# Optimization experiments

Hardware: AMD Instinct MI355X
Metric: run time of the kernel (lower is better)

The kernel has to match this reference:

```python
import jax, jax.numpy as jnp
import numpy as np


def setup_inputs() -> dict:
    key = jax.random.key(0)
    ks = jax.random.split(key, 6)
    N, T, D, H = 256, 128, 512, 512
    x = jax.random.normal(ks[0], (N, T, D), dtype=jnp.float32)
    A = jax.random.normal(ks[1], (N, H, 4, 4), dtype=jnp.float32)
    Wx = jax.random.normal(ks[2], (D, 4 * H), dtype=jnp.float32) / np.sqrt(D)
    Wh = jax.random.normal(ks[3], (H, 4 * H), dtype=jnp.float32) / np.sqrt(H)
    Wattn = jax.random.normal(ks[4], (H, 4 * H), dtype=jnp.float32) / np.sqrt(H)
    b = jnp.zeros((4 * H,), dtype=jnp.float32)
    return {"x": x, "A": A, "Wx": Wx, "Wh": Wh, "Wattn": Wattn, "b": b}


def reference(x, A, Wx, Wh, Wattn, b):
    N, T, D = x.shape
    H = Wh.shape[0]
    A_flat = A.reshape(N, H, -1)  # (N, H, 16)
    h0 = A_flat.mean(axis=-1)     # mean over 4x4 grid
    c0 = h0
    inv_sqrt_H = 1.0 / np.sqrt(H).astype(np.float32)

    def step(carry, x_t):
        h, c = carry
        # scaled dot-product attention over the 16 spatial cells
        scores = jnp.einsum('nh,nhp->np', h, A_flat) * inv_sqrt_H  # (N, 16)
        w = jax.nn.softmax(scores, axis=-1)
        attn = jnp.einsum('nhp,np->nh', A_flat, w)                 # (N, H)
        a = x_t @ Wx + h @ Wh + attn @ Wattn + b                   # (N, 4H)
        a_i, a_f, a_o, a_g = jnp.split(a, 4, axis=1)
        i = jax.nn.sigmoid(a_i)
        f = jax.nn.sigmoid(a_f)
        o = jax.nn.sigmoid(a_o)
        g = jnp.tanh(a_g)
        c_next = f * c + i * g
        h_next = o * jnp.tanh(c_next)
        return (h_next, c_next), h_next

    _, hs = jax.lax.scan(step, (h0, c0), jnp.swapaxes(x, 0, 1))  # (T, N, H)
    return jnp.swapaxes(hs, 0, 1)  # (N, T, H)
```

## Files before the change

kernel.cpp:

```cpp
#include <hip/hip_runtime.h>
#include <math.h>

typedef unsigned short u16;
typedef _Float16 h16;
typedef _Float16 f16x8 __attribute__((ext_vector_type(8)));
typedef float f32x4 __attribute__((ext_vector_type(4)));

__device__ __forceinline__ float sigm(float x) { return 1.f / (1.f + expf(-x)); }


__global__ void k_pack_w(const float* __restrict__ Wx, const float* __restrict__ Wh,
                         h16* __restrict__ WhiS, h16* __restrict__ WloS) {
  unsigned idx = blockIdx.x * 256 + threadIdx.x;
  unsigned e = idx & 7, l = (idx >> 3) & 63, cf = (idx >> 9) & 1;
  unsigned t2 = idx >> 10;
  unsigned j = t2 >> 5, ks = t2 & 31;
  unsigned k = ks * 32 + ((l >> 4) << 3) + e;
  unsigned c32 = cf * 16 + (l & 15);
  unsigned acol = (c32 >> 3) * 512 + j * 8 + (c32 & 7);
  float v = (k < 512) ? Wx[(size_t)k * 2048 + acol]
                      : Wh[(size_t)(k - 512) * 2048 + acol];
  h16 hi = (h16)v;
  WhiS[idx] = hi;
  WloS[idx] = (h16)((v - (float)hi) * 4096.f);
}

__global__ __launch_bounds__(256) void k_m(const float* __restrict__ Af,
                                           const float* __restrict__ Wat,
                                           float* __restrict__ M2) {
  __shared__ float Alds[8192];
  const int tid = threadIdx.x;
  const int cb = blockIdx.x;
  const int n  = blockIdx.y;
  {
    const float4* src = (const float4*)(Af + (size_t)n * 8192);
    float4* dst = (float4*)Alds;
    for (int i = tid; i < 2048; i += 256) dst[i] = src[i];
  }
  __syncthreads();
  const int c0 = cb * 512 + tid * 2;
  float acc0[16], acc1[16];
#pragma unroll
  for (int p = 0; p < 16; ++p) { acc0[p] = 0.f; acc1[p] = 0.f; }
  for (int k = 0; k < 512; ++k) {
    float2 wv2 = *(const float2*)(Wat + (size_t)k * 2048 + c0);
    const float* ar = Alds + k * 16;
#pragma unroll
    for (int p = 0; p < 16; ++p) {
      acc0[p] += ar[p] * wv2.x;
      acc1[p] += ar[p] * wv2.y;
    }
  }
  float* o = M2 + ((size_t)n * 2048 + c0) * 16;
#pragma unroll
  for (int p = 0; p < 16; ++p) { o[p] = acc0[p]; o[16 + p] = acc1[p]; }
}

__global__ void k_xsplit(const float* __restrict__ x, h16* __restrict__ xhi,
                         h16* __restrict__ xlo) {
  size_t i = ((size_t)blockIdx.x * 256 + threadIdx.x) * 4;
  float4 v = *(const float4*)(x + i);
  union { h16 h[4]; uint2 u; } a, b;
  float vv[4] = {v.x, v.y, v.z, v.w};
#pragma unroll
  for (int e = 0; e < 4; ++e) {
    h16 hh = (h16)vv[e];
    a.h[e] = hh;
    b.h[e] = (h16)((vv[e] - (float)hh) * 4096.f);
  }
  *(uint2*)(xhi + i) = a.u;
  *(uint2*)(xlo + i) = b.u;
}

__global__ __launch_bounds__(512) void k_init(const float* __restrict__ Af,
                                              h16* __restrict__ hhi,
                                              h16* __restrict__ hlo,
                                              float* __restrict__ cst,
                                              float* __restrict__ sb0) {
  const int n = blockIdx.x, k = threadIdx.x;
  float Areg[16];
  const f32x4* A4 = (const f32x4*)(Af + (size_t)n * 8192 + k * 16);
#pragma unroll
  for (int q4 = 0; q4 < 4; ++q4) {
    f32x4 v = A4[q4];
#pragma unroll
    for (int e = 0; e < 4; ++e) Areg[q4 * 4 + e] = v[e];
  }
  float s = 0.f;
#pragma unroll
  for (int p = 0; p < 16; ++p) s += Areg[p];
  s *= 0.0625f;
  const int idx = n * 512 + k;
  cst[idx] = s;
  h16 hh = (h16)s;
  hhi[idx] = hh;
  hlo[idx] = (h16)((s - (float)hh) * 4096.f);
  float ps[16];
#pragma unroll
  for (int p = 0; p < 16; ++p) ps[p] = s * Areg[p];
#pragma unroll
  for (int m = 1; m <= 4; m <<= 1)
#pragma unroll
    for (int p = 0; p < 16; ++p) ps[p] += __shfl_xor(ps[p], m);
  if ((k & 7) == 0) {
    float* o = sb0 + ((size_t)n * 64 + (k >> 3)) * 16;
#pragma unroll
    for (int p = 0; p < 16; ++p) o[p] = ps[p];
  }
}

template<bool XPRE>
__global__ __launch_bounds__(512, 4) void k_step(
    const float* __restrict__ bv, const float* __restrict__ Af,
    const float* __restrict__ x, const h16* __restrict__ xhi, const h16* __restrict__ xlo,
    const h16* __restrict__ WhiS, const h16* __restrict__ WloS,
    const float* __restrict__ Mws,
    const float* __restrict__ sbR, float* __restrict__ sbW,
    h16* __restrict__ hhi, h16* __restrict__ hlo,
    float* __restrict__ cst, float* __restrict__ out, int t) {
  __shared__ float P[7 * 1056];
  __shared__ float wsh[32][17];

  const int tid = threadIdx.x;
  const int l = tid & 63, wv = tid >> 6;
  const int bid = blockIdx.x;
  const int g = bid >> 6;
  const int j = (bid & 7) * 8 + ((bid >> 3) & 7);
  const int n0 = g * 32;
  const int rA = n0 + (l & 15);
  const int klane = (l >> 4) * 8;

  {
    const int nS = tid >> 4, pS = tid & 15;
    const float* sr = sbR + ((size_t)(n0 + nS) * 64) * 16 + pS;
    float s = 0.f;
#pragma unroll 8
    for (int jj = 0; jj < 64; ++jj) s += sr[jj * 16];
    s *= 0.04419417382415922f;
    float m = s;
#pragma unroll
    for (int o = 8; o >= 1; o >>= 1) m = fmaxf(m, __shfl_xor(m, o, 16));
    float e = __expf(s - m);
    float se = e;
#pragma unroll
    for (int o = 8; o >= 1; o >>= 1) se += __shfl_xor(se, o, 16);
    wsh[nS][pS] = e / se;
  }

  const h16* whiJ = WhiS + (size_t)j * 32768;
  const h16* wloJ = WloS + (size_t)j * 32768;

  const int rC = tid >> 3, qC = tid & 7;
  const int colC = j * 8 + qC;
  const float b_i = bv[colC], b_f = bv[512 + colC], b_o = bv[1024 + colC],
              b_g = bv[1536 + colC];

  const int rb = t & 1, wb = rb ^ 1;
  const h16* hhiR = hhi + (size_t)rb * 131072;
  const h16* hloR = hlo + (size_t)rb * 131072;

  f32x4 acc1[2][2], acc2[2][2];
#pragma unroll
  for (int rt = 0; rt < 2; ++rt)
#pragma unroll
    for (int cf = 0; cf < 2; ++cf) {
      acc1[rt][cf] = (f32x4){0.f, 0.f, 0.f, 0.f};
      acc2[rt][cf] = (f32x4){0.f, 0.f, 0.f, 0.f};
    }

  auto kstep = [&](int ksg) {
    const f16x8 bh0 = *(const f16x8*)(whiJ + ((size_t)(ksg * 2 + 0) * 64 + l) * 8);
    const f16x8 bh1 = *(const f16x8*)(whiJ + ((size_t)(ksg * 2 + 1) * 64 + l) * 8);
    const f16x8 bl0 = *(const f16x8*)(wloJ + ((size_t)(ksg * 2 + 0) * 64 + l) * 8);
    const f16x8 bl1 = *(const f16x8*)(wloJ + ((size_t)(ksg * 2 + 1) * 64 + l) * 8);
    f16x8 Ah[2], Al[2];
    const int kg = ksg * 32;
    if (kg < 512) {
      const size_t base = ((size_t)rA * 128 + t) * 512 + kg + klane;
      if (XPRE) {
#pragma unroll
        for (int rt = 0; rt < 2; ++rt) {
          Ah[rt] = *(const f16x8*)(xhi + base + (size_t)rt * 1048576);
          Al[rt] = *(const f16x8*)(xlo + base + (size_t)rt * 1048576);
        }
      } else {
#pragma unroll
        for (int rt = 0; rt < 2; ++rt) {
          const float* xp = x + base + (size_t)rt * 1048576;
          f32x4 v0 = *(const f32x4*)xp, v1 = *(const f32x4*)(xp + 4);
          float vv[8] = {v0[0], v0[1], v0[2], v0[3], v1[0], v1[1], v1[2], v1[3]};
#pragma unroll
          for (int e = 0; e < 8; ++e) {
            h16 hh = (h16)vv[e];
            Ah[rt][e] = hh;
            Al[rt][e] = (h16)((vv[e] - (float)hh) * 4096.f);
          }
        }
      }
    } else {
      const size_t base = (size_t)rA * 512 + (kg - 512) + klane;
#pragma unroll
      for (int rt = 0; rt < 2; ++rt) {
        Ah[rt] = *(const f16x8*)(hhiR + base + rt * 8192);
        Al[rt] = *(const f16x8*)(hloR + base + rt * 8192);
      }
    }
#pragma unroll
    for (int rt = 0; rt < 2; ++rt) {
      acc1[rt][0] = __builtin_amdgcn_mfma_f32_16x16x32_f16(Ah[rt], bh0, acc1[rt][0], 0, 0, 0);
      acc1[rt][1] = __builtin_amdgcn_mfma_f32_16x16x32_f16(Ah[rt], bh1, acc1[rt][1], 0, 0, 0);
      acc2[rt][0] = __builtin_amdgcn_mfma_f32_16x16x32_f16(Al[rt], bh0, acc2[rt][0], 0, 0, 0);
      acc2[rt][1] = __builtin_amdgcn_mfma_f32_16x16x32_f16(Al[rt], bh1, acc2[rt][1], 0, 0, 0);
      acc2[rt][0] = __builtin_amdgcn_mfma_f32_16x16x32_f16(Ah[rt], bl0, acc2[rt][0], 0, 0, 0);
      acc2[rt][1] = __builtin_amdgcn_mfma_f32_16x16x32_f16(Ah[rt], bl1, acc2[rt][1], 0, 0, 0);
    }
  };

#pragma unroll
  for (int i = 0; i < 4; ++i) kstep(wv + 8 * i);

  float accf[2][2][4];
#pragma unroll
  for (int rt = 0; rt < 2; ++rt)
#pragma unroll
    for (int cf = 0; cf < 2; ++cf)
#pragma unroll
      for (int rg = 0; rg < 4; ++rg)
        accf[rt][cf][rg] = acc1[rt][cf][rg] + acc2[rt][cf][rg] * (1.f / 4096.f);

  auto publish = [&](int slot) {
#pragma unroll
    for (int rt = 0; rt < 2; ++rt)
#pragma unroll
      for (int cf = 0; cf < 2; ++cf)
#pragma unroll
        for (int rg = 0; rg < 4; ++rg)
          P[slot * 1056 + (rt * 16 + (l >> 4) * 4 + rg) * 33 + cf * 16 + (l & 15)] =
              accf[rt][cf][rg];
  };
  auto addin = [&](int slot) {
#pragma unroll
    for (int rt = 0; rt < 2; ++rt)
#pragma unroll
      for (int cf = 0; cf < 2; ++cf)
#pragma unroll
        for (int rg = 0; rg < 4; ++rg)
          accf[rt][cf][rg] +=
              P[slot * 1056 + (rt * 16 + (l >> 4) * 4 + rg) * 33 + cf * 16 + (l & 15)];
  };

  if (wv >= 4) publish(wv - 4);
  __syncthreads();
  if (wv < 4) addin(wv);
  if (wv == 2) publish(4);
  if (wv == 3) publish(5);
  __syncthreads();
  if (wv == 0) addin(4);
  if (wv == 1) { addin(5); publish(6); }
  __syncthreads();
  if (wv == 0) { addin(6); publish(0); }
  __syncthreads();

  if (tid < 256) {
    const float* Mr = Mws + ((size_t)(n0 + rC) * 2048 + colC) * 16;
    float am[4];
#pragma unroll
    for (int f = 0; f < 4; ++f) {
      const float* mp = Mr + (size_t)f * 8192;
      float s = 0.f;
#pragma unroll
      for (int p = 0; p < 16; ++p) s += wsh[rC][p] * mp[p];
      am[f] = s;
    }
    float ai = P[rC * 33 + qC] + am[0] + b_i;
    float af_ = P[rC * 33 + 8 + qC] + am[1] + b_f;
    float ao = P[rC * 33 + 16 + qC] + am[2] + b_o;
    float ag = P[rC * 33 + 24 + qC] + am[3] + b_g;
    float ig = sigm(ai), fg = sigm(af_), og = sigm(ao), gg = tanhf(ag);
    const size_t cix = (size_t)(n0 + rC) * 512 + colC;
    float c = cst[cix];
    float cn = fg * c + ig * gg;
    cst[cix] = cn;
    float hn = og * tanhf(cn);
    h16 hh = (h16)hn;
    hhi[(size_t)wb * 131072 + cix] = hh;
    hlo[(size_t)wb * 131072 + cix] = (h16)((hn - (float)hh) * 4096.f);
    out[((size_t)(n0 + rC) * 128 + t) * 512 + colC] = hn;

    float Areg[16];
    const f32x4* A4 = (const f32x4*)(Af + ((size_t)(n0 + rC) * 512 + colC) * 16);
#pragma unroll
    for (int q4 = 0; q4 < 4; ++q4) {
      f32x4 v = A4[q4];
#pragma unroll
      for (int e = 0; e < 4; ++e) Areg[q4 * 4 + e] = v[e];
    }
    float ps[16];
#pragma unroll
    for (int p = 0; p < 16; ++p) ps[p] = hn * Areg[p];
#pragma unroll
    for (int m = 1; m <= 4; m <<= 1)
#pragma unroll
      for (int p = 0; p < 16; ++p) ps[p] += __shfl_xor(ps[p], m);
    if (qC == 0) {
      float* o = sbW + ((size_t)(n0 + rC) * 64 + j) * 16;
#pragma unroll
      for (int p = 0; p < 16; ++p) o[p] = ps[p];
    }
  }
}


extern "C" void kernel_launch(void* const* d_in, const int* in_sizes, int n_in,
                              void* d_out, int out_size, void* d_ws, size_t ws_size,
                              hipStream_t stream) {
  (void)in_sizes; (void)n_in; (void)out_size;
  const float* x   = (const float*)d_in[0];
  const float* Af  = (const float*)d_in[1];
  const float* Wx  = (const float*)d_in[2];
  const float* Wh  = (const float*)d_in[3];
  const float* Wat = (const float*)d_in[4];
  const float* bv  = (const float*)d_in[5];
  float* out = (float*)d_out;

  char* ws = (char*)d_ws;
  size_t off = 0;
  auto alloc = [&](size_t nb) {
    char* p = ws + off; off = (off + nb + 255) & ~(size_t)255; return p;
  };
  h16*   WhiS = (h16*)alloc(2097152ull * 2);
  h16*   WloS = (h16*)alloc(2097152ull * 2);
  float* Mws  = (float*)alloc(8388608ull * 4);
  float* sb   = (float*)alloc(2ull * 262144 * 4);
  h16*   hhi  = (h16*)alloc(262144ull * 2);
  h16*   hlo  = (h16*)alloc(262144ull * 2);
  float* cst  = (float*)alloc(131072ull * 4);
  size_t base_end = off;
  h16* xhi = (h16*)alloc(16777216ull * 2);
  h16* xlo = (h16*)alloc(16777216ull * 2);
  bool xpre = (ws_size >= base_end + 2ull * 16777216ull * 2 + 4096);

  k_pack_w<<<8192, 256, 0, stream>>>(Wx, Wh, WhiS, WloS);
  k_m<<<dim3(4, 256), 256, 0, stream>>>(Af, Wat, Mws);
  k_init<<<256, 512, 0, stream>>>(Af, hhi, hlo, cst, sb);
  if (xpre) k_xsplit<<<16384, 256, 0, stream>>>(x, xhi, xlo);

  for (int t = 0; t < 128; ++t) {
    const float* sbR = sb + (size_t)(t & 1) * 262144;
    float* sbW = (float*)sb + (size_t)((t + 1) & 1) * 262144;
    if (xpre)
      k_step<true><<<512, 512, 0, stream>>>(bv, Af, x, xhi, xlo, WhiS, WloS, Mws,
                                            sbR, sbW, hhi, hlo, cst, out, t);
    else
      k_step<false><<<512, 512, 0, stream>>>(bv, Af, x, xhi, xlo, WhiS, WloS, Mws,
                                             sbR, sbW, hhi, hlo, cst, out, t);
  }
}
```

Baseline: 2.785 ms.

## Pre-swizzle x and h into MFMA fragment layout and use MFMA for attention projection

Stores the fp16 hi/lo splits of x and h in a fragment-major layout, so each lane of a k_step wave reads one contiguous 16-byte chunk and the wave reads one contiguous block, instead of strided row accesses. The k_m precompute of the attention projection is rewritten to use split-fp16 MFMA over a larger grid in place of scalar FMA loops. Writers in k_init, k_xsplit and the step epilogue now use the matching swizzled indices. The cost is more complex index arithmetic and a scattered 2-byte write pattern for h.

New measurement: 2.261 ms. 18.8% less time.

```diff
diff --git a/kernel.cpp b/kernel.cpp
--- a/kernel.cpp
+++ b/kernel.cpp
@@ -30,7 +30,7 @@
                                            float* __restrict__ M2) {
   __shared__ float Alds[8192];
   const int tid = threadIdx.x;
-  const int cb = blockIdx.x;
+  const int ct = blockIdx.x;
   const int n  = blockIdx.y;
   {
     const float4* src = (const float4*)(Af + (size_t)n * 8192);
@@ -38,43 +38,58 @@
     for (int i = tid; i < 2048; i += 256) dst[i] = src[i];
   }
   __syncthreads();
-  const int c0 = cb * 512 + tid * 2;
-  float acc0[16], acc1[16];
-#pragma unroll
-  for (int p = 0; p < 16; ++p) { acc0[p] = 0.f; acc1[p] = 0.f; }
-  for (int k = 0; k < 512; ++k) {
-    float2 wv2 = *(const float2*)(Wat + (size_t)k * 2048 + c0);
-    const float* ar = Alds + k * 16;
-#pragma unroll
-    for (int p = 0; p < 16; ++p) {
-      acc0[p] += ar[p] * wv2.x;
-      acc1[p] += ar[p] * wv2.y;
-    }
-  }
-  float* o = M2 + ((size_t)n * 2048 + c0) * 16;
-#pragma unroll
-  for (int p = 0; p < 16; ++p) { o[p] = acc0[p]; o[16 + p] = acc1[p]; }
-}
-
-__global__ void k_xsplit(const float* __restrict__ x, h16* __restrict__ xhi,
-                         h16* __restrict__ xlo) {
-  size_t i = ((size_t)blockIdx.x * 256 + threadIdx.x) * 4;
-  float4 v = *(const float4*)(x + i);
-  union { h16 h[4]; uint2 u; } a, b;
-  float vv[4] = {v.x, v.y, v.z, v.w};
-#pragma unroll
-  for (int e = 0; e < 4; ++e) {
+  const int l = tid & 63, w = tid >> 6;
+  const int col = ct * 64 + w * 16 + (l & 15);
+  const int lq = l >> 4;
+  f32x4 acc1 = {0.f, 0.f, 0.f, 0.f}, acc2 = {0.f, 0.f, 0.f, 0.f};
+  for (int k0 = 0; k0 < 512; k0 += 32) {
+    float av[8], wv[8];
+#pragma unroll
+    for (int e = 0; e < 8; ++e) av[e] = Alds[(k0 + lq * 8 + e) * 16 + (l & 15)];
+#pragma unroll
+    for (int e = 0; e < 8; ++e) wv[e] = Wat[(size_t)(k0 + lq * 8 + e) * 2048 + col];
+    f16x8 Ah, Al_, Bh, Bl;
+#pragma unroll
+    for (int e = 0; e < 8; ++e) {
+      h16 ah = (h16)av[e]; Ah[e] = ah; Al_[e] = (h16)((av[e] - (float)ah) * 4096.f);
+      h16 bh = (h16)wv[e]; Bh[e] = bh; Bl[e]  = (h16)((wv[e] - (float)bh) * 4096.f);
+    }
+    acc1 = __builtin_amdgcn_mfma_f32_16x16x32_f16(Ah, Bh, acc1, 0, 0, 0);
+    acc2 = __builtin_amdgcn_mfma_f32_16x16x32_f16(Al_, Bh, acc2, 0, 0, 0);
+    acc2 = __builtin_amdgcn_mfma_f32_16x16x32_f16(Ah, Bl, acc2, 0, 0, 0);
+  }
+  float4 o;
+  o.x = acc1[0] + acc2[0] * (1.f / 4096.f);
+  o.y = acc1[1] + acc2[1] * (1.f / 4096.f);
+  o.z = acc1[2] + acc2[2] * (1.f / 4096.f);
+  o.w = acc1[3] + acc2[3] * (1.f / 4096.f);
+  *(float4*)(M2 + ((size_t)n * 2048 + col) * 16 + lq * 4) = o;
+}
+
+__global__ void k_xsplit(const float* __restrict__ x, h16* __restrict__ xfhi,
+                         h16* __restrict__ xflo) {
+  unsigned tg = blockIdx.x * 256 + threadIdx.x;
+  unsigned l = tg & 63, rt = (tg >> 6) & 1, ksg = (tg >> 7) & 15;
+  unsigned g = (tg >> 11) & 7, t = tg >> 14;
+  int n = g * 32 + rt * 16 + (l & 15);
+  int k0 = ksg * 32 + (l >> 4) * 8;
+  const float* xp = x + ((size_t)n * 128 + t) * 512 + k0;
+  f32x4 v0 = *(const f32x4*)xp, v1 = *(const f32x4*)(xp + 4);
+  float vv[8] = {v0[0], v0[1], v0[2], v0[3], v1[0], v1[1], v1[2], v1[3]};
+  union { h16 h[8]; uint4 u; } a, b;
+#pragma unroll
+  for (int e = 0; e < 8; ++e) {
     h16 hh = (h16)vv[e];
     a.h[e] = hh;
     b.h[e] = (h16)((vv[e] - (float)hh) * 4096.f);
   }
-  *(uint2*)(xhi + i) = a.u;
-  *(uint2*)(xlo + i) = b.u;
+  *(uint4*)(xfhi + (size_t)tg * 8) = a.u;
+  *(uint4*)(xflo + (size_t)tg * 8) = b.u;
 }
 
 __global__ __launch_bounds__(512) void k_init(const float* __restrict__ Af,
-                                              h16* __restrict__ hhi,
-                                              h16* __restrict__ hlo,
+                                              h16* __restrict__ hfhi,
+                                              h16* __restrict__ hflo,
                                               float* __restrict__ cst,
                                               float* __restrict__ sb0) {
   const int n = blockIdx.x, k = threadIdx.x;
@@ -90,11 +105,13 @@
 #pragma unroll
   for (int p = 0; p < 16; ++p) s += Areg[p];
   s *= 0.0625f;
-  const int idx = n * 512 + k;
-  cst[idx] = s;
+  cst[n * 512 + k] = s;
   h16 hh = (h16)s;
-  hhi[idx] = hh;
-  hlo[idx] = (h16)((s - (float)hh) * 4096.f);
+  const int g = n >> 5;
+  const int hoff = ((((g * 16 + (k >> 5)) * 2 + ((n >> 4) & 1)) * 64 +
+                     ((n & 15) | (((k >> 3) & 3) << 4))) * 8) + (k & 7);
+  hfhi[hoff] = hh;
+  hflo[hoff] = (h16)((s - (float)hh) * 4096.f);
   float ps[16];
 #pragma unroll
   for (int p = 0; p < 16; ++p) ps[p] = s * Areg[p];
@@ -112,11 +129,11 @@
 template<bool XPRE>
 __global__ __launch_bounds__(512, 4) void k_step(
     const float* __restrict__ bv, const float* __restrict__ Af,
-    const float* __restrict__ x, const h16* __restrict__ xhi, const h16* __restrict__ xlo,
+    const float* __restrict__ x, const h16* __restrict__ xfhi, const h16* __restrict__ xflo,
     const h16* __restrict__ WhiS, const h16* __restrict__ WloS,
     const float* __restrict__ Mws,
     const float* __restrict__ sbR, float* __restrict__ sbW,
-    h16* __restrict__ hhi, h16* __restrict__ hlo,
+    h16* __restrict__ hfhi, h16* __restrict__ hflo,
     float* __restrict__ cst, float* __restrict__ out, int t) {
   __shared__ float P[7 * 1056];
   __shared__ float wsh[32][17];
@@ -127,8 +144,6 @@
   const int g = bid >> 6;
   const int j = (bid & 7) * 8 + ((bid >> 3) & 7);
   const int n0 = g * 32;
-  const int rA = n0 + (l & 15);
-  const int klane = (l >> 4) * 8;
 
   {
     const int nS = tid >> 4, pS = tid & 15;
@@ -156,8 +171,8 @@
               b_g = bv[1536 + colC];
 
   const int rb = t & 1, wb = rb ^ 1;
-  const h16* hhiR = hhi + (size_t)rb * 131072;
-  const h16* hloR = hlo + (size_t)rb * 131072;
+  const h16* hfhiR = hfhi + (size_t)rb * 131072;
+  const h16* hfloR = hflo + (size_t)rb * 131072;
 
   f32x4 acc1[2][2], acc2[2][2];
 #pragma unroll
@@ -174,19 +189,20 @@
     const f16x8 bl0 = *(const f16x8*)(wloJ + ((size_t)(ksg * 2 + 0) * 64 + l) * 8);
     const f16x8 bl1 = *(const f16x8*)(wloJ + ((size_t)(ksg * 2 + 1) * 64 + l) * 8);
     f16x8 Ah[2], Al[2];
-    const int kg = ksg * 32;
-    if (kg < 512) {
-      const size_t base = ((size_t)rA * 128 + t) * 512 + kg + klane;
+    if (ksg < 16) {
       if (XPRE) {
 #pragma unroll
         for (int rt = 0; rt < 2; ++rt) {
-          Ah[rt] = *(const f16x8*)(xhi + base + (size_t)rt * 1048576);
-          Al[rt] = *(const f16x8*)(xlo + base + (size_t)rt * 1048576);
+          const size_t base = ((((size_t)t * 8 + g) * 16 + ksg) * 2 + rt) * 512 + l * 8;
+          Ah[rt] = *(const f16x8*)(xfhi + base);
+          Al[rt] = *(const f16x8*)(xflo + base);
         }
       } else {
 #pragma unroll
         for (int rt = 0; rt < 2; ++rt) {
-          const float* xp = x + base + (size_t)rt * 1048576;
+          const int n_x = g * 32 + rt * 16 + (l & 15);
+          const int k_x = ksg * 32 + (l >> 4) * 8;
+          const float* xp = x + ((size_t)n_x * 128 + t) * 512 + k_x;
           f32x4 v0 = *(const f32x4*)xp, v1 = *(const f32x4*)(xp + 4);
           float vv[8] = {v0[0], v0[1], v0[2], v0[3], v1[0], v1[1], v1[2], v1[3]};
 #pragma unroll
@@ -198,11 +214,11 @@
         }
       }
     } else {
-      const size_t base = (size_t)rA * 512 + (kg - 512) + klane;
 #pragma unroll
       for (int rt = 0; rt < 2; ++rt) {
-        Ah[rt] = *(const f16x8*)(hhiR + base + rt * 8192);
-        Al[rt] = *(const f16x8*)(hloR + base + rt * 8192);
+        const size_t base = (((size_t)(g * 16 + (ksg - 16)) * 2 + rt) * 64 + l) * 8;
+        Ah[rt] = *(const f16x8*)(hfhiR + base);
+        Al[rt] = *(const f16x8*)(hfloR + base);
       }
     }
 #pragma unroll
@@ -283,8 +299,10 @@
     cst[cix] = cn;
     float hn = og * tanhf(cn);
     h16 hh = (h16)hn;
-    hhi[(size_t)wb * 131072 + cix] = hh;
-    hlo[(size_t)wb * 131072 + cix] = (h16)((hn - (float)hh) * 4096.f);
+    const int hoff = ((((g * 16 + (j >> 2)) * 2 + (rC >> 4)) * 64 +
+                       ((rC & 15) | ((j & 3) << 4))) * 8) + qC;
+    hfhi[(size_t)wb * 131072 + hoff] = hh;
+    hflo[(size_t)wb * 131072 + hoff] = (h16)((hn - (float)hh) * 4096.f);
     out[((size_t)(n0 + rC) * 128 + t) * 512 + colC] = hn;
 
     float Areg[16];
@@ -332,27 +350,27 @@
   h16*   WloS = (h16*)alloc(2097152ull * 2);
   float* Mws  = (float*)alloc(8388608ull * 4);
   float* sb   = (float*)alloc(2ull * 262144 * 4);
-  h16*   hhi  = (h16*)alloc(262144ull * 2);
-  h16*   hlo  = (h16*)alloc(262144ull * 2);
+  h16*   hfhi = (h16*)alloc(262144ull * 2);
+  h16*   hflo = (h16*)alloc(262144ull * 2);
   float* cst  = (float*)alloc(131072ull * 4);
   size_t base_end = off;
-  h16* xhi = (h16*)alloc(16777216ull * 2);
-  h16* xlo = (h16*)alloc(16777216ull * 2);
+  h16* xfhi = (h16*)alloc(16777216ull * 2);
+  h16* xflo = (h16*)alloc(16777216ull * 2);
   bool xpre = (ws_size >= base_end + 2ull * 16777216ull * 2 + 4096);
 
   k_pack_w<<<8192, 256, 0, stream>>>(Wx, Wh, WhiS, WloS);
-  k_m<<<dim3(4, 256), 256, 0, stream>>>(Af, Wat, Mws);
-  k_init<<<256, 512, 0, stream>>>(Af, hhi, hlo, cst, sb);
-  if (xpre) k_xsplit<<<16384, 256, 0, stream>>>(x, xhi, xlo);
+  k_m<<<dim3(32, 256), 256, 0, stream>>>(Af, Wat, Mws);
+  k_init<<<256, 512, 0, stream>>>(Af, hfhi, hflo, cst, sb);
+  if (xpre) k_xsplit<<<8192, 256, 0, stream>>>(x, xfhi, xflo);
 
   for (int t = 0; t < 128; ++t) {
     const float* sbR = sb + (size_t)(t & 1) * 262144;
     float* sbW = (float*)sb + (size_t)((t + 1) & 1) * 262144;
     if (xpre)
-      k_step<true><<<512, 512, 0, stream>>>(bv, Af, x, xhi, xlo, WhiS, WloS, Mws,
-                                            sbR, sbW, hhi, hlo, cst, out, t);
+      k_step<true><<<512, 512, 0, stream>>>(bv, Af, x, xfhi, xflo, WhiS, WloS, Mws,
+                                            sbR, sbW, hfhi, hflo, cst, out, t);
     else
-      k_step<false><<<512, 512, 0, stream>>>(bv, Af, x, xhi, xlo, WhiS, WloS, Mws,
-                                             sbR, sbW, hhi, hlo, cst, out, t);
-  }
-}
+      k_step<false><<<512, 512, 0, stream>>>(bv, Af, x, xfhi, xflo, WhiS, WloS, Mws,
+                                             sbR, sbW, hfhi, hflo, cst, out, t);
+  }
+}
```
